# Optimization experiments

Hardware: AMD Instinct MI355X
Metric: run time of the kernel (lower is better)

## Reference

```python
import jax, jax.numpy as jnp
import numpy as np

D = 1024
H = 16
HD = D // H
FF = 4 * D
EPS = 1e-5


def _ln(x, g, b):
    mu = jnp.mean(x, axis=-1, keepdims=True)
    var = jnp.mean(jnp.square(x - mu), axis=-1, keepdims=True)
    return (x - mu) * jax.lax.rsqrt(var + EPS) * g + b


def setup_inputs() -> dict:
    key = jax.random.key(0)
    ks = jax.random.split(key, 16)
    s = 0.02
    return {
        "x": jax.random.normal(ks[0], (2, 2048, D), dtype=jnp.float32),
        "g1": jnp.ones((D,), jnp.float32),
        "b1": jnp.zeros((D,), jnp.float32),
        "Wqkv": jax.random.normal(ks[1], (D, 3 * D), jnp.float32) * s,
        "bqkv": jnp.zeros((3 * D,), jnp.float32),
        "Wo": jax.random.normal(ks[2], (D, D), jnp.float32) * s,
        "bo": jnp.zeros((D,), jnp.float32),
        "g2": jnp.ones((D,), jnp.float32),
        "b2": jnp.zeros((D,), jnp.float32),
        "W1": jax.random.normal(ks[3], (D, FF), jnp.float32) * s,
        "b1f": jnp.zeros((FF,), jnp.float32),
        "W2": jax.random.normal(ks[4], (FF, D), jnp.float32) * s,
        "b2f": jnp.zeros((D,), jnp.float32),
    }


def reference(x, g1, b1, Wqkv, bqkv, Wo, bo, g2, b2, W1, b1f, W2, b2f):
    b, t, d = x.shape
    residual = x
    h = _ln(x, g1, b1)
    qkv = (h @ Wqkv + bqkv).reshape(b, t, 3, H, HD)
    q, k, v = [jnp.transpose(qkv[:, :, i], (0, 2, 1, 3)) for i in range(3)]  # (b,h,t,hd)
    scale = 1.0 / np.sqrt(HD).astype(np.float32)
    attn = jnp.einsum("bhqd,bhkd->bhqk", q, k) * scale
    # cache_offset = 0 in offline mode: mask = (j < 0) | (j <= i) -> causal
    i = jnp.arange(t)[:, None]
    j = jnp.arange(t)[None, :]
    mask = j <= i
    attn = jnp.where(mask, attn, -jnp.inf)
    attn = jax.nn.softmax(attn, axis=-1)
    out = jnp.einsum("bhqk,bhkd->bhqd", attn, v)
    out = jnp.transpose(out, (0, 2, 1, 3)).reshape(b, t, d)
    x = residual + out @ Wo + bo
    hh = _ln(x, g2, b2)
    ff = jax.nn.gelu(hh @ W1 + b1f, approximate=False) @ W2 + b2f
    return x + ff
```

## Files before the change

### kernel.cpp

```cpp
#include <hip/hip_runtime.h>
#include <math.h>

#define TD 1024
#define NH 16
#define HDIM 64
#define SEQ 2048
#define NB 2
#define NROWS 4096
#define FFD 4096

#define QSCALE 0.18033688011112042f

typedef unsigned short u16;
typedef __attribute__((ext_vector_type(8))) short bf16x8;
typedef __attribute__((ext_vector_type(4))) float f32x4;

__device__ __forceinline__ u16 f2bf(float f) {
    union { float f; unsigned u; } v; v.f = f;
    return (u16)((v.u + 0x7FFFu + ((v.u >> 16) & 1u)) >> 16);
}

__device__ __forceinline__ void async16(void* lds, const void* g) {
    __builtin_amdgcn_global_load_lds(
        (const __attribute__((address_space(1))) unsigned*)g,
        (__attribute__((address_space(3))) unsigned*)lds, 16, 0, 0);
}

__device__ __forceinline__ float gelu_f(float v) {
    float u = 0.7978845608028654f * (v + 0.044715f * v * v * v);
    float e = __expf(2.f * u);
    float th = 1.f - 2.f * __builtin_amdgcn_rcpf(e + 1.f);
    return 0.5f * v * (1.f + th);
}

__global__ __launch_bounds__(256) void ln_bf16(const float* __restrict__ x,
                                               const float* __restrict__ g,
                                               const float* __restrict__ b,
                                               u16* __restrict__ out)
{
    int row = blockIdx.x;
    const float* xr = x + (size_t)row * TD;
    u16* outr = out + (size_t)row * TD;
    int t = threadIdx.x;
    float v[4];
    float s = 0.f, ss = 0.f;
#pragma unroll
    for (int i = 0; i < 4; i++) {
        v[i] = xr[t + 256 * i];
        s += v[i];
        ss += v[i] * v[i];
    }
#pragma unroll
    for (int o = 32; o > 0; o >>= 1) {
        s  += __shfl_down(s, o);
        ss += __shfl_down(ss, o);
    }
    __shared__ float sm[4], sm2[4];
    int wave = t >> 6, lane = t & 63;
    if (lane == 0) { sm[wave] = s; sm2[wave] = ss; }
    __syncthreads();
    s  = sm[0] + sm[1] + sm[2] + sm[3];
    ss = sm2[0] + sm2[1] + sm2[2] + sm2[3];
    float mu  = s * (1.f / TD);
    float var = ss * (1.f / TD) - mu * mu;
    float rstd = rsqrtf(var + 1e-5f);
#pragma unroll
    for (int i = 0; i < 4; i++) {
        int c = t + 256 * i;
        outr[c] = f2bf((v[i] - mu) * rstd * g[c] + b[c]);
    }
}

__global__ __launch_bounds__(256) void prep_kernel(
    const float* __restrict__ Wqkv, const float* __restrict__ Wo,
    const float* __restrict__ W1,   const float* __restrict__ W2,
    u16* __restrict__ wqkvT, u16* __restrict__ woT,
    u16* __restrict__ w1T,   u16* __restrict__ w2T,
    const float* __restrict__ x, const float* __restrict__ g1,
    const float* __restrict__ b1, u16* __restrict__ hbuf)
{
    int blk = blockIdx.x;
    int t = threadIdx.x;
    if (blk >= 3072) {
        int row = blk - 3072;
        const float* xr = x + (size_t)row * TD;
        u16* outr = hbuf + (size_t)row * TD;
        float v[4];
        float s = 0.f, ss = 0.f;
#pragma unroll
        for (int i = 0; i < 4; i++) {
            v[i] = xr[t + 256 * i];
            s += v[i];
            ss += v[i] * v[i];
        }
#pragma unroll
        for (int o = 32; o > 0; o >>= 1) {
            s  += __shfl_down(s, o);
            ss += __shfl_down(ss, o);
        }
        __shared__ float sm[4], sm2[4];
        int wave = t >> 6, lane = t & 63;
        if (lane == 0) { sm[wave] = s; sm2[wave] = ss; }
        __syncthreads();
        s  = sm[0] + sm[1] + sm[2] + sm[3];
        ss = sm2[0] + sm2[1] + sm2[2] + sm2[3];
        float mu  = s * (1.f / TD);
        float var = ss * (1.f / TD) - mu * mu;
        float rstd = rsqrtf(var + 1e-5f);
#pragma unroll
        for (int i = 0; i < 4; i++) {
            int c = t + 256 * i;
            outr[c] = f2bf((v[i] - mu) * rstd * g1[c] + b1[c]);
        }
        return;
    }
    const float* W; u16* Wt; int K, N, local, nx;
    if (blk < 768)       { W = Wqkv; Wt = wqkvT; K = TD;  N = 3 * TD; local = blk;        nx = 48; }
    else if (blk < 1024) { W = Wo;   Wt = woT;   K = TD;  N = TD;     local = blk - 768;  nx = 16; }
    else if (blk < 2048) { W = W1;   Wt = w1T;   K = TD;  N = FFD;    local = blk - 1024; nx = 64; }
    else                 { W = W2;   Wt = w2T;   K = FFD; N = TD;     local = blk - 2048; nx = 16; }
    int n0 = (local % nx) * 64, k0 = (local / nx) * 64;
    __shared__ u16 tile[64][65];
    int c = t & 63, rq = t >> 6;
#pragma unroll
    for (int i = 0; i < 16; i++) {
        int r = rq * 16 + i;
        tile[r][c] = f2bf(W[(size_t)(k0 + r) * N + n0 + c]);
    }
    __syncthreads();
#pragma unroll
    for (int i = 0; i < 16; i++) {
        int r = rq * 16 + i;
        Wt[(size_t)(n0 + r) * K + k0 + c] = tile[c][r];
    }
}

#define EPI_QKV 0
#define EPI_F32RES 1
#define EPI_GELU 2

template<int EPI, int TN, int BK>
__global__ __launch_bounds__(256) void gemm_mfma(int M, int N, int K,
    const u16* __restrict__ A, const u16* __restrict__ Bt,
    const float* __restrict__ bias, const float* __restrict__ res,
    float* __restrict__ Cf, u16* __restrict__ Cb,
    u16* __restrict__ qb, u16* __restrict__ kb, u16* __restrict__ vb)
{
    constexpr int WN  = TN / 2;
    constexpr int NJ  = WN / 16;
    constexpr int KH  = BK / 32;
    constexpr int CPR = BK / 8;
    constexpr int ACH = (128 * CPR) / 256;
    constexpr int BCH = (TN  * CPR) / 256;
    constexpr int ASZ = 128 * BK * 2;
    constexpr int BSZ = TN  * BK * 2;
    __shared__ __align__(16) char smem[2 * (ASZ + BSZ)];

    int t = threadIdx.x;
    int lane = t & 63, w = t >> 6;
    int wm = w >> 1, wn = w & 1;
    int lr = lane & 15, lq = lane >> 4;
    int gx = gridDim.x;
    int lin = blockIdx.x + gx * blockIdx.y;
    int li = lin >> 3;
    int qy = li / gx;
    int ty = (lin & 7) * (gridDim.y >> 3) + qy;
    int tx = li - qy * gx;
    int m0 = ty * 128, n0 = tx * TN;
    int pg = (lq ^ (lr & (CPR - 1))) * 16;

    const u16* ap[ACH];
    const u16* bp[BCH];
#pragma unroll
    for (int i = 0; i < ACH; i++) {
        int c = t + 256 * i, r = c / CPR, s = c % CPR;
        int g = s ^ (r & (CPR - 1));
        ap[i] = A + (size_t)(m0 + r) * K + g * 8;
    }
#pragma unroll
    for (int i = 0; i < BCH; i++) {
        int c = t + 256 * i, r = c / CPR, s = c % CPR;
        int g = s ^ (r & (CPR - 1));
        bp[i] = Bt + (size_t)(n0 + r) * K + g * 8;
    }

    f32x4 acc[4][NJ];
#pragma unroll
    for (int i = 0; i < 4; i++)
#pragma unroll
        for (int j = 0; j < NJ; j++) acc[i][j] = (f32x4){0.f, 0.f, 0.f, 0.f};

#pragma unroll
    for (int i = 0; i < ACH; i++)
        async16(smem + (t + 256 * i) * 16, ap[i]);
#pragma unroll
    for (int i = 0; i < BCH; i++)
        async16(smem + 2 * ASZ + (t + 256 * i) * 16, bp[i]);

    int nk = K / BK;
    for (int kt = 0; kt < nk; kt++) {
        int cur = kt & 1;
        __syncthreads();
        if (kt + 1 < nk) {
            char* An = smem + (1 - cur) * ASZ;
            char* Bn = smem + 2 * ASZ + (1 - cur) * BSZ;
#pragma unroll
            for (int i = 0; i < ACH; i++) {
                ap[i] += BK;
                async16(An + (t + 256 * i) * 16, ap[i]);
            }
#pragma unroll
            for (int i = 0; i < BCH; i++) {
                bp[i] += BK;
                async16(Bn + (t + 256 * i) * 16, bp[i]);
            }
        }
        const char* Ac = smem + cur * ASZ;
        const char* Bc = smem + 2 * ASZ + cur * BSZ;
#pragma unroll
        for (int h = 0; h < KH; h++) {
            bf16x8 af[4], bfr[NJ];
#pragma unroll
            for (int i = 0; i < 4; i++)
                af[i] = *(const bf16x8*)(Ac + (wm * 64 + i * 16 + lr) * (2 * BK) + (pg ^ (h * 64)));
#pragma unroll
            for (int j = 0; j < NJ; j++)
                bfr[j] = *(const bf16x8*)(Bc + (wn * WN + j * 16 + lr) * (2 * BK) + (pg ^ (h * 64)));
#pragma unroll
            for (int i = 0; i < 4; i++)
#pragma unroll
                for (int j = 0; j < NJ; j++)
                    acc[i][j] = __builtin_amdgcn_mfma_f32_16x16x32_bf16(af[i], bfr[j], acc[i][j], 0, 0, 0);
        }
    }

#pragma unroll
    for (int i = 0; i < 4; i++) {
        int rowb = m0 + wm * 64 + i * 16 + lq * 4;
#pragma unroll
        for (int j = 0; j < NJ; j++) {
            int col = n0 + wn * WN + j * 16 + lr;
            float bs = bias[col];
            float vals[4];
#pragma unroll
            for (int r = 0; r < 4; r++) vals[r] = acc[i][j][r] + bs;
            if (EPI == EPI_F32RES) {
#pragma unroll
                for (int r = 0; r < 4; r++) {
                    int rr = rowb + r;
                    Cf[(size_t)rr * N + col] = vals[r] + res[(size_t)rr * N + col];
                }
            } else if (EPI == EPI_GELU) {
#pragma unroll
                for (int r = 0; r < 4; r++)
                    Cb[(size_t)(rowb + r) * N + col] = f2bf(gelu_f(vals[r]));
            } else {
                int comp = col >> 10, cw = col & 1023;
                int h = cw >> 6, d = cw & 63;
                int bb0 = rowb >> 11, ts = rowb & 2047;
                int bh = bb0 * NH + h;
                if (comp == 0) {
#pragma unroll
                    for (int r = 0; r < 4; r++)
                        qb[((size_t)bh * SEQ + ts + r) * HDIM + d] = f2bf(vals[r] * QSCALE);
                } else if (comp == 1) {
#pragma unroll
                    for (int r = 0; r < 4; r++)
                        kb[((size_t)bh * SEQ + ts + r) * HDIM + d] = f2bf(vals[r]);
                } else {
                    ushort4 pk;
                    pk.x = f2bf(vals[0]); pk.y = f2bf(vals[1]);
                    pk.z = f2bf(vals[2]); pk.w = f2bf(vals[3]);
                    *(ushort4*)&vb[((size_t)bh * HDIM + d) * SEQ + ts] = pk;
                }
            }
        }
    }
}

__global__ __launch_bounds__(256, 4) void attn_mfma(const u16* __restrict__ qb,
                                                    const u16* __restrict__ kb,
                                                    const u16* __restrict__ vb,
                                                    u16* __restrict__ ctx)
{
    __shared__ __align__(16) char smem[40960];
    char* QP = smem;
    int lin = blockIdx.x + 32 * blockIdx.y;
    int xcd = lin & 7, idx = lin >> 3;
    int u = idx & 31, v = idx >> 5;
    int bh = xcd + 8 * v;
    int qt = (v & 1) ? u : 31 - u;
    int bb = bh >> 4, h = bh & 15;
    int t = threadIdx.x, lane = t & 63, w = t >> 6;
    int lr = lane & 15, lq = lane >> 4;
    int sw = (lr & 7) * 16;
    int cA = (lq * 16) ^ sw;
    int cB = (64 | (lq * 16)) ^ sw;
    int c0 = t,        r0 = c0 >> 3, g0 = (c0 & 7) ^ (r0 & 7);
    int c1 = t + 256,  r1 = c1 >> 3, g1 = (c1 & 7) ^ (r1 & 7);
    size_t off0  = (size_t)r0 * 128  + g0 * 16;
    size_t off1  = (size_t)r1 * 128  + g1 * 16;
    size_t voff0 = (size_t)r0 * 4096 + g0 * 16;
    size_t voff1 = (size_t)r1 * 4096 + g1 * 16;

    const char* qg_base = (const char*)qb + (size_t)bh * SEQ * 128;
    const char* kg_base = (const char*)kb + (size_t)bh * SEQ * 128;
    const char* vg_base = (const char*)vb + (size_t)bh * 64 * 4096;

    const char* qg = qg_base + (size_t)qt * 8192;
    async16(QP + c0 * 16, qg + off0);
    async16(QP + c1 * 16, qg + off1);
    async16(smem + 8192 + c0 * 16, kg_base + off0);
    async16(smem + 8192 + c1 * 16, kg_base + off1);
    async16(smem + 24576 + c0 * 16, vg_base + voff0);
    async16(smem + 24576 + c1 * 16, vg_base + voff1);

    float mold = -INFINITY, lsum = 0.f;
    f32x4 o[4];
#pragma unroll
    for (int dj = 0; dj < 4; dj++) o[dj] = (f32x4){0.f, 0.f, 0.f, 0.f};
    bf16x8 bq0, bq1;

    for (int kt = 0; kt <= qt; ++kt) {
        int cur = kt & 1;
        __syncthreads();
        if (kt < qt) {
            const char* kgn = kg_base + (size_t)(kt + 1) * 8192;
            const char* vgn = vg_base + (size_t)(kt + 1) * 128;
            char* Kn = smem + 8192  + (1 - cur) * 8192;
            char* Vn = smem + 24576 + (1 - cur) * 8192;
            async16(Kn + c0 * 16, kgn + off0);
            async16(Kn + c1 * 16, kgn + off1);
            async16(Vn + c0 * 16, vgn + voff0);
            async16(Vn + c1 * 16, vgn + voff1);
        }
        if (kt == 0) {
            const char* qr = QP + (w * 16 + lr) * 128;
            bq0 = *(const bf16x8*)(qr + cA);
            bq1 = *(const bf16x8*)(qr + cB);
        }
        const char* Kc = smem + 8192  + cur * 8192;
        const char* Vc = smem + 24576 + cur * 8192;

        float sv[4][4];
        bool diag = (kt == qt);
        __builtin_amdgcn_s_setprio(1);
#pragma unroll
        for (int j = 0; j < 4; ++j) {
            const char* kr = Kc + (j * 16 + lr) * 128;
            bf16x8 ak0 = *(const bf16x8*)(kr + cA);
            bf16x8 ak1 = *(const bf16x8*)(kr + cB);
            f32x4 z = (f32x4){0.f, 0.f, 0.f, 0.f};
            z = __builtin_amdgcn_mfma_f32_16x16x32_bf16(ak0, bq0, z, 0, 0, 0);
            z = __builtin_amdgcn_mfma_f32_16x16x32_bf16(ak1, bq1, z, 0, 0, 0);
#pragma unroll
            for (int r = 0; r < 4; r++) {
                float xv = z[r];
                if (diag && (j * 16 + lq * 4 + r > w * 16 + lr)) xv = -INFINITY;
                sv[j][r] = xv;
            }
        }
        __builtin_amdgcn_s_setprio(0);
        float mx = sv[0][0];
#pragma unroll
        for (int j = 0; j < 4; j++)
#pragma unroll
            for (int r = 0; r < 4; r++) mx = fmaxf(mx, sv[j][r]);
        mx = fmaxf(mx, __shfl_xor(mx, 16));
        mx = fmaxf(mx, __shfl_xor(mx, 32));
        float mnew = fmaxf(mold, mx);
        float alpha = exp2f(mold - mnew);
        float rs = 0.f;
        unsigned pk[4][2];
#pragma unroll
        for (int j = 0; j < 4; j++)
#pragma unroll
            for (int hh = 0; hh < 2; hh++) {
                float p0 = exp2f(sv[j][2 * hh]     - mnew);
                float p1 = exp2f(sv[j][2 * hh + 1] - mnew);
                rs += p0 + p1;
                union { float f; unsigned u; } a0, a1;
                a0.f = p0; a1.f = p1;
                pk[j][hh] = __builtin_amdgcn_perm(a1.u, a0.u, 0x07060302u);
            }
        rs += __shfl_xor(rs, 16);
        rs += __shfl_xor(rs, 32);
        lsum = lsum * alpha + rs;
        mold = mnew;
#pragma unroll
        for (int dj = 0; dj < 4; dj++)
#pragma unroll
            for (int r = 0; r < 4; r++) o[dj][r] *= alpha;

        {
            char* pw = QP + (w * 16 + lr) * 128 + (lq & 1) * 8;
#pragma unroll
            for (int j = 0; j < 4; j++) {
                int pos = ((j * 2 + (lq >> 1)) * 16) ^ sw;
                uint2 u2; u2.x = pk[j][0]; u2.y = pk[j][1];
                *(uint2*)(pw + pos) = u2;
            }
        }
        asm volatile("s_waitcnt lgkmcnt(0)" ::: "memory");
        const char* pr = QP + (w * 16 + lr) * 128;
        bf16x8 bp0 = *(const bf16x8*)(pr + cA);
        bf16x8 bp1 = *(const bf16x8*)(pr + cB);
        __builtin_amdgcn_s_setprio(1);
#pragma unroll
        for (int dj = 0; dj < 4; ++dj) {
            const char* vr = Vc + (dj * 16 + lr) * 128;
            bf16x8 av0 = *(const bf16x8*)(vr + cA);
            bf16x8 av1 = *(const bf16x8*)(vr + cB);
            o[dj] = __builtin_amdgcn_mfma_f32_16x16x32_bf16(av0, bp0, o[dj], 0, 0, 0);
            o[dj] = __builtin_amdgcn_mfma_f32_16x16x32_bf16(av1, bp1, o[dj], 0, 0, 0);
        }
        __builtin_amdgcn_s_setprio(0);
    }

    float inv = 1.f / lsum;
    int tok = qt * 64 + w * 16 + lr;
    u16* cp = ctx + ((size_t)(bb * SEQ) + tok) * TD + h * HDIM + lq * 4;
#pragma unroll
    for (int dj = 0; dj < 4; dj++) {
        ushort4 s4;
        s4.x = f2bf(o[dj][0] * inv); s4.y = f2bf(o[dj][1] * inv);
        s4.z = f2bf(o[dj][2] * inv); s4.w = f2bf(o[dj][3] * inv);
        *(ushort4*)(cp + dj * 16) = s4;
    }
}

extern "C" void kernel_launch(void* const* d_in, const int* in_sizes, int n_in,
                              void* d_out, int out_size, void* d_ws, size_t ws_size,
                              hipStream_t stream)
{
    const float* x    = (const float*)d_in[0];
    const float* g1   = (const float*)d_in[1];
    const float* b1   = (const float*)d_in[2];
    const float* Wqkv = (const float*)d_in[3];
    const float* bqkv = (const float*)d_in[4];
    const float* Wo   = (const float*)d_in[5];
    const float* bo   = (const float*)d_in[6];
    const float* g2   = (const float*)d_in[7];
    const float* b2   = (const float*)d_in[8];
    const float* W1   = (const float*)d_in[9];
    const float* b1f  = (const float*)d_in[10];
    const float* W2   = (const float*)d_in[11];
    const float* b2f  = (const float*)d_in[12];
    float* out = (float*)d_out;

    char* ws = (char*)d_ws;
    const size_t MB = 1ull << 20;
    u16* wqkvT = (u16*)(ws + 0 * MB);
    u16* woT   = (u16*)(ws + 6 * MB);
    u16* w1T   = (u16*)(ws + 8 * MB);
    u16* w2T   = (u16*)(ws + 16 * MB);
    u16* qbuf  = (u16*)(ws + 24 * MB);
    u16* kbuf  = (u16*)(ws + 32 * MB);
    u16* vbuf  = (u16*)(ws + 40 * MB);
    u16* hbuf  = (u16*)(ws + 48 * MB);
    u16* ctx   = (u16*)(ws + 56 * MB);
    float* x2  = (float*)(ws + 64 * MB);
    u16* ff1   = (u16*)(ws + 80 * MB);

    prep_kernel<<<3072 + NROWS, 256, 0, stream>>>(
        Wqkv, Wo, W1, W2, wqkvT, woT, w1T, w2T, x, g1, b1, hbuf);

    gemm_mfma<EPI_QKV, 128, 32><<<dim3(3 * TD / 128, NROWS / 128), 256, 0, stream>>>(
        NROWS, 3 * TD, TD, hbuf, wqkvT, bqkv, nullptr, nullptr, nullptr, qbuf, kbuf, vbuf);
    attn_mfma<<<dim3(32, NB * NH), 256, 0, stream>>>(qbuf, kbuf, vbuf, ctx);
    gemm_mfma<EPI_F32RES, 64, 64><<<dim3(TD / 64, NROWS / 128), 256, 0, stream>>>(
        NROWS, TD, TD, ctx, woT, bo, x, x2, nullptr, nullptr, nullptr, nullptr);
    ln_bf16<<<NROWS, 256, 0, stream>>>(x2, g2, b2, hbuf);
    gemm_mfma<EPI_GELU, 128, 32><<<dim3(FFD / 128, NROWS / 128), 256, 0, stream>>>(
        NROWS, FFD, TD, hbuf, w1T, b1f, nullptr, nullptr, ff1, nullptr, nullptr, nullptr);
    gemm_mfma<EPI_F32RES, 64, 64><<<dim3(TD / 64, NROWS / 128), 256, 0, stream>>>(
        NROWS, TD, FFD, ff1, w2T, b2f, x2, out, nullptr, nullptr, nullptr, nullptr);
}
```

Measured before the change: 309.1 us.

## Add triple-buffered async LDS pipeline with explicit vmcnt waits for wide GEMMs

```diff
diff --git a/kernel.cpp b/kernel.cpp
--- a/kernel.cpp
+++ b/kernel.cpp
@@ -139,7 +139,7 @@
 #define EPI_F32RES 1
 #define EPI_GELU 2
 
-template<int EPI, int TN, int BK>
+template<int EPI, int TN, int BK, int NBUF>
 __global__ __launch_bounds__(256) void gemm_mfma(int M, int N, int K,
     const u16* __restrict__ A, const u16* __restrict__ Bt,
     const float* __restrict__ bias, const float* __restrict__ res,
@@ -154,7 +154,7 @@
     constexpr int BCH = (TN  * CPR) / 256;
     constexpr int ASZ = 128 * BK * 2;
     constexpr int BSZ = TN  * BK * 2;
-    __shared__ __align__(16) char smem[2 * (ASZ + BSZ)];
+    __shared__ __align__(16) char smem[NBUF * (ASZ + BSZ)];
 
     int t = threadIdx.x;
     int lane = t & 63, w = t >> 6;
@@ -190,47 +190,113 @@
 #pragma unroll
         for (int j = 0; j < NJ; j++) acc[i][j] = (f32x4){0.f, 0.f, 0.f, 0.f};
 
-#pragma unroll
-    for (int i = 0; i < ACH; i++)
-        async16(smem + (t + 256 * i) * 16, ap[i]);
-#pragma unroll
-    for (int i = 0; i < BCH; i++)
-        async16(smem + 2 * ASZ + (t + 256 * i) * 16, bp[i]);
-
     int nk = K / BK;
-    for (int kt = 0; kt < nk; kt++) {
-        int cur = kt & 1;
-        __syncthreads();
-        if (kt + 1 < nk) {
-            char* An = smem + (1 - cur) * ASZ;
-            char* Bn = smem + 2 * ASZ + (1 - cur) * BSZ;
+
+    if constexpr (NBUF == 2) {
+#pragma unroll
+        for (int i = 0; i < ACH; i++)
+            async16(smem + (t + 256 * i) * 16, ap[i]);
+#pragma unroll
+        for (int i = 0; i < BCH; i++)
+            async16(smem + 2 * ASZ + (t + 256 * i) * 16, bp[i]);
+
+        for (int kt = 0; kt < nk; kt++) {
+            int cur = kt & 1;
+            __syncthreads();
+            if (kt + 1 < nk) {
+                char* An = smem + (1 - cur) * ASZ;
+                char* Bn = smem + 2 * ASZ + (1 - cur) * BSZ;
+#pragma unroll
+                for (int i = 0; i < ACH; i++) {
+                    ap[i] += BK;
+                    async16(An + (t + 256 * i) * 16, ap[i]);
+                }
+#pragma unroll
+                for (int i = 0; i < BCH; i++) {
+                    bp[i] += BK;
+                    async16(Bn + (t + 256 * i) * 16, bp[i]);
+                }
+            }
+            const char* Ac = smem + cur * ASZ;
+            const char* Bc = smem + 2 * ASZ + cur * BSZ;
+#pragma unroll
+            for (int h = 0; h < KH; h++) {
+                bf16x8 af[4], bfr[NJ];
+#pragma unroll
+                for (int i = 0; i < 4; i++)
+                    af[i] = *(const bf16x8*)(Ac + (wm * 64 + i * 16 + lr) * (2 * BK) + (pg ^ (h * 64)));
+#pragma unroll
+                for (int j = 0; j < NJ; j++)
+                    bfr[j] = *(const bf16x8*)(Bc + (wn * WN + j * 16 + lr) * (2 * BK) + (pg ^ (h * 64)));
+#pragma unroll
+                for (int i = 0; i < 4; i++)
+#pragma unroll
+                    for (int j = 0; j < NJ; j++)
+                        acc[i][j] = __builtin_amdgcn_mfma_f32_16x16x32_bf16(af[i], bfr[j], acc[i][j], 0, 0, 0);
+            }
+        }
+    } else {
+        static_assert(NBUF == 3, "only depth 2/3 implemented");
+        static_assert(ACH + BCH == 4, "vmcnt immediates assume 4 loads/slab");
+#pragma unroll
+        for (int s = 0; s < NBUF; s++) {
+            char* Ab = smem + s * ASZ;
+            char* Bb = smem + NBUF * ASZ + s * BSZ;
 #pragma unroll
             for (int i = 0; i < ACH; i++) {
+                async16(Ab + (t + 256 * i) * 16, ap[i]);
                 ap[i] += BK;
-                async16(An + (t + 256 * i) * 16, ap[i]);
             }
 #pragma unroll
             for (int i = 0; i < BCH; i++) {
+                async16(Bb + (t + 256 * i) * 16, bp[i]);
                 bp[i] += BK;
-                async16(Bn + (t + 256 * i) * 16, bp[i]);
-            }
-        }
-        const char* Ac = smem + cur * ASZ;
-        const char* Bc = smem + 2 * ASZ + cur * BSZ;
-#pragma unroll
-        for (int h = 0; h < KH; h++) {
-            bf16x8 af[4], bfr[NJ];
-#pragma unroll
-            for (int i = 0; i < 4; i++)
-                af[i] = *(const bf16x8*)(Ac + (wm * 64 + i * 16 + lr) * (2 * BK) + (pg ^ (h * 64)));
-#pragma unroll
-            for (int j = 0; j < NJ; j++)
-                bfr[j] = *(const bf16x8*)(Bc + (wn * WN + j * 16 + lr) * (2 * BK) + (pg ^ (h * 64)));
-#pragma unroll
-            for (int i = 0; i < 4; i++)
+            }
+        }
+        for (int kt = 0; kt < nk; kt++) {
+            int cur = kt % NBUF;
+            int rem = nk - 1 - kt;
+            if (rem >= 2)      asm volatile("s_waitcnt vmcnt(8)" ::: "memory");
+            else if (rem == 1) asm volatile("s_waitcnt vmcnt(4)" ::: "memory");
+            else               asm volatile("s_waitcnt vmcnt(0)" ::: "memory");
+            __builtin_amdgcn_sched_barrier(0);
+            __builtin_amdgcn_s_barrier();
+            __builtin_amdgcn_sched_barrier(0);
+            const char* Ac = smem + cur * ASZ;
+            const char* Bc = smem + NBUF * ASZ + cur * BSZ;
+#pragma unroll
+            for (int h = 0; h < KH; h++) {
+                bf16x8 af[4], bfr[NJ];
+#pragma unroll
+                for (int i = 0; i < 4; i++)
+                    af[i] = *(const bf16x8*)(Ac + (wm * 64 + i * 16 + lr) * (2 * BK) + (pg ^ (h * 64)));
 #pragma unroll
                 for (int j = 0; j < NJ; j++)
-                    acc[i][j] = __builtin_amdgcn_mfma_f32_16x16x32_bf16(af[i], bfr[j], acc[i][j], 0, 0, 0);
+                    bfr[j] = *(const bf16x8*)(Bc + (wn * WN + j * 16 + lr) * (2 * BK) + (pg ^ (h * 64)));
+#pragma unroll
+                for (int i = 0; i < 4; i++)
+#pragma unroll
+                    for (int j = 0; j < NJ; j++)
+                        acc[i][j] = __builtin_amdgcn_mfma_f32_16x16x32_bf16(af[i], bfr[j], acc[i][j], 0, 0, 0);
+            }
+            asm volatile("s_waitcnt lgkmcnt(0)" ::: "memory");
+            __builtin_amdgcn_sched_barrier(0);
+            __builtin_amdgcn_s_barrier();
+            __builtin_amdgcn_sched_barrier(0);
+            if (kt + NBUF < nk) {
+                char* An = smem + cur * ASZ;
+                char* Bn = smem + NBUF * ASZ + cur * BSZ;
+#pragma unroll
+                for (int i = 0; i < ACH; i++) {
+                    async16(An + (t + 256 * i) * 16, ap[i]);
+                    ap[i] += BK;
+                }
+#pragma unroll
+                for (int i = 0; i < BCH; i++) {
+                    async16(Bn + (t + 256 * i) * 16, bp[i]);
+                    bp[i] += BK;
+                }
+            }
         }
     }
 
@@ -465,14 +531,14 @@
     prep_kernel<<<3072 + NROWS, 256, 0, stream>>>(
         Wqkv, Wo, W1, W2, wqkvT, woT, w1T, w2T, x, g1, b1, hbuf);
 
-    gemm_mfma<EPI_QKV, 128, 32><<<dim3(3 * TD / 128, NROWS / 128), 256, 0, stream>>>(
+    gemm_mfma<EPI_QKV, 128, 32, 3><<<dim3(3 * TD / 128, NROWS / 128), 256, 0, stream>>>(
         NROWS, 3 * TD, TD, hbuf, wqkvT, bqkv, nullptr, nullptr, nullptr, qbuf, kbuf, vbuf);
     attn_mfma<<<dim3(32, NB * NH), 256, 0, stream>>>(qbuf, kbuf, vbuf, ctx);
-    gemm_mfma<EPI_F32RES, 64, 64><<<dim3(TD / 64, NROWS / 128), 256, 0, stream>>>(
+    gemm_mfma<EPI_F32RES, 64, 64, 2><<<dim3(TD / 64, NROWS / 128), 256, 0, stream>>>(
         NROWS, TD, TD, ctx, woT, bo, x, x2, nullptr, nullptr, nullptr, nullptr);
     ln_bf16<<<NROWS, 256, 0, stream>>>(x2, g2, b2, hbuf);
-    gemm_mfma<EPI_GELU, 128, 32><<<dim3(FFD / 128, NROWS / 128), 256, 0, stream>>>(
+    gemm_mfma<EPI_GELU, 128, 32, 3><<<dim3(FFD / 128, NROWS / 128), 256, 0, stream>>>(
         NROWS, FFD, TD, hbuf, w1T, b1f, nullptr, nullptr, ff1, nullptr, nullptr, nullptr);
-    gemm_mfma<EPI_F32RES, 64, 64><<<dim3(TD / 64, NROWS / 128), 256, 0, stream>>>(
+    gemm_mfma<EPI_F32RES, 64, 64, 2><<<dim3(TD / 64, NROWS / 128), 256, 0, stream>>>(
         NROWS, TD, FFD, ff1, w2T, b2f, x2, out, nullptr, nullptr, nullptr, nullptr);
 }
```

Measured after the change: 315.8 us. 1.02x slower.
